# Optimization experiments

Measured on AMD Instinct MI355X. Metric: run time of the kernel, lower is better.

## Reference

```python
import jax, jax.numpy as jnp
import numpy as np

B, LQ, LD = 64, 20, 512
D, NB, WIN = 300, 11, 5
EQ, ED, DESC, KC = 5, 10, 20, 10
VW, VE, VC = 50000, 10000, 5000

# KNRM kernel centers / widths (requires_grad=False buffers in the original)
MU = jnp.array([1.0, 0.9, 0.7, 0.5, 0.3, 0.1, -0.1, -0.3, -0.5, -0.7, -0.9], jnp.float32)
SIGMA = jnp.array([1e-3] + [0.1] * 10, jnp.float32)


def setup_inputs() -> dict:
    key = jax.random.key(0)
    ks = jax.random.split(key, 20)
    f = lambda k, s, sc: jax.random.normal(k, s, jnp.float32) * sc
    return {
        "inputs_qwt": jax.random.randint(ks[0], (B, LQ), 0, VW),
        "inputs_qwm": jnp.ones((B, LQ), jnp.float32),
        "inputs_qei": jax.random.randint(ks[1], (B, EQ), 0, VE),
        "inputs_qet": jax.random.randint(ks[2], (B, EQ * DESC), 0, VW),
        "inputs_qew": jax.random.randint(ks[3], (B, EQ * KC), 0, VC),
        "inputs_qem": jnp.ones((B, EQ), jnp.float32),
        "inputs_dwt": jax.random.randint(ks[4], (B, LD), 0, VW),
        "inputs_dwm": jnp.ones((B, LD), jnp.float32),
        "inputs_dei": jax.random.randint(ks[5], (B, ED), 0, VE),
        "inputs_det": jax.random.randint(ks[6], (B, ED * DESC), 0, VW),
        "inputs_dew": jax.random.randint(ks[7], (B, ED * KC), 0, VC),
        "inputs_dem": jnp.ones((B, ED), jnp.float32),
        "wrd_emb": f(ks[8], (VW, D), 0.1),
        "ent_emb": f(ks[9], (VE, 128), 0.1),
        "car_emb": f(ks[10], (VC, 128), 0.1),
        "bow_W": f(ks[11], (128, D), 0.05), "bow_b": jnp.zeros((128,), jnp.float32),
        "conv_uni_W": f(ks[12], (128, 1, D), 0.05), "conv_uni_b": jnp.zeros((128,), jnp.float32),
        "conv_bi_W": f(ks[13], (128, 2, D), 0.04), "conv_bi_b": jnp.zeros((128,), jnp.float32),
        "conv_tri_W": f(ks[14], (128, 3, D), 0.03), "conv_tri_b": jnp.zeros((128,), jnp.float32),
        "conv_des_W": f(ks[15], (128, WIN, D), 0.02), "conv_des_b": jnp.zeros((128,), jnp.float32),
        "dense_f_W": f(ks[16], (1, 16 * NB), 0.1), "dense_f_b": jnp.zeros((1,), jnp.float32),
    }


def _conv_words(x, w, b):
    # x: [N, L, D]; w: [O, k, D] -> relu conv over the word axis, valid padding -> [N, L-k+1, O]
    k, L = w.shape[1], x.shape[1]
    segs = jnp.stack([x[:, i:L - k + 1 + i] for i in range(k)], axis=2)  # [N, L-k+1, k, D]
    return jax.nn.relu(jnp.einsum('nlkd,okd->nlo', segs, w) + b)


def _l2(x):
    return x / jnp.maximum(jnp.linalg.norm(x, axis=-1, keepdims=True), 1e-10)


def _kernel_pool(q, d, mq, md):
    # q:[B,Lq,128] d:[B,Ld,128] mq:[B,Lq] md:[B,Ld] -> [B, NB]
    sim = jnp.einsum('bqe,bde->bqd', q, d)
    pv = jnp.exp(-0.5 * (sim[..., None] - MU) ** 2 / (SIGMA ** 2)) * md[:, None, :, None]
    lps = jnp.log(jnp.maximum(pv.sum(2), 1e-10)) * 0.01 * mq[:, :, None]
    return lps.sum(1)


def _forward(inputs_qwt, inputs_qwm, inputs_qei, inputs_qet, inputs_qew, inputs_qem,
             inputs_dwt, inputs_dwm, inputs_dei, inputs_det, inputs_dew, inputs_dem,
             wrd_emb, ent_emb, car_emb, bow_W, bow_b,
             conv_uni_W, conv_uni_b, conv_bi_W, conv_bi_b, conv_tri_W, conv_tri_b,
             conv_des_W, conv_des_b, dense_f_W, dense_f_b):
    b = inputs_qwt.shape[0]
    qw = wrd_emb[inputs_qwt]  # [B, LQ, D]
    dw = wrd_emb[inputs_dwt]  # [B, LD, D]

    def ent_branch(ids_e, ids_desc, ids_car, n_ent, w_bow):
        desc = wrd_emb[ids_desc].reshape(b * n_ent, DESC, D)
        e_conv = _conv_words(desc, conv_des_W, conv_des_b).max(1).reshape(b, n_ent, 128)
        t = car_emb[ids_car].reshape(b, n_ent * KC, 128)
        att = jax.nn.softmax((w_bow * t).sum(2).reshape(b, n_ent, KC, 1), axis=2)
        ew = (att * t.reshape(b, n_ent, KC, 128)).sum(2)
        return ent_emb[ids_e] + e_conv + ew

    qw_bow = (jnp.einsum('bld,od->blo', qw, bow_W) + bow_b).sum(1, keepdims=True)  # [B,1,128]
    dw_bow = (jnp.einsum('bld,od->blo', dw, bow_W) + bow_b).sum(1, keepdims=True)
    qs = _l2(ent_branch(inputs_qei, inputs_qet, inputs_qew, EQ, qw_bow))  # [B,5,128]
    ds = _l2(ent_branch(inputs_dei, inputs_det, inputs_dew, ED, dw_bow))  # [B,10,128]

    qu = _l2(_conv_words(qw, conv_uni_W, conv_uni_b))
    qb = _l2(_conv_words(qw, conv_bi_W, conv_bi_b))
    qt = _l2(_conv_words(qw, conv_tri_W, conv_tri_b))
    du = _l2(_conv_words(dw, conv_uni_W, conv_uni_b))
    db = _l2(_conv_words(dw, conv_bi_W, conv_bi_b))
    dt = _l2(_conv_words(dw, conv_tri_W, conv_tri_b))

    mqu, mqb, mqt = inputs_qwm, inputs_qwm[:, :-1], inputs_qwm[:, :-2]
    mdu, mdb, mdt = inputs_dwm, inputs_dwm[:, :-1], inputs_dwm[:, :-2]

    kp = _kernel_pool
    pools = [kp(qu, du, mqu, mdu), kp(qu, dt, mqu, mdt), kp(qu, db, mqu, mdb),
             kp(qb, du, mqb, mdu), kp(qt, du, mqt, mdu), kp(qb, db, mqb, mdb),
             kp(qb, dt, mqb, mdt), kp(qt, db, mqt, mdb), kp(qt, dt, mqt, mdt),
             kp(qs, du, inputs_qem, mdu), kp(qs, db, inputs_qem, mdb), kp(qs, dt, inputs_qem, mdt),
             kp(qu, ds, mqu, inputs_dem), kp(qb, ds, mqb, inputs_dem), kp(qt, ds, mqt, inputs_dem),
             kp(qs, ds, inputs_qem, inputs_dem)]
    feats = jnp.concatenate(pools, axis=1)  # [B, 16*NB]
    return jnp.tanh(feats @ dense_f_W.T + dense_f_b)[:, 0]


def reference(inputs_qwt, inputs_qwm, inputs_qei, inputs_qet, inputs_qew, inputs_qem,
              inputs_dwt, inputs_dwm, inputs_dei, inputs_det, inputs_dew, inputs_dem,
              wrd_emb, ent_emb, car_emb, bow_W, bow_b,
              conv_uni_W, conv_uni_b, conv_bi_W, conv_bi_b, conv_tri_W, conv_tri_b,
              conv_des_W, conv_des_b, dense_f_W, dense_f_b):
    return _forward(inputs_qwt, inputs_qwm, inputs_qei, inputs_qet, inputs_qew, inputs_qem,
                    inputs_dwt, inputs_dwm, inputs_dei, inputs_det, inputs_dew, inputs_dem,
                    wrd_emb, ent_emb, car_emb, bow_W, bow_b,
                    conv_uni_W, conv_uni_b, conv_bi_W, conv_bi_b, conv_tri_W, conv_tri_b,
                    conv_des_W, conv_des_b, dense_f_W, dense_f_b)
```

## Files before the change

kernel.cpp:

```cpp
#include <hip/hip_runtime.h>

typedef unsigned short u16;
typedef unsigned int u32;
typedef __attribute__((ext_vector_type(8))) short bf16x8;
typedef __attribute__((ext_vector_type(4))) float f32x4;

#define DEVI __device__ __forceinline__

namespace {
constexpr int LQ_ = 20, LD_ = 512, D_ = 300;
constexpr int EQ_ = 5, ED_ = 10, KC_ = 10;
constexpr int QROWS = 62, DROWS = 1543;
constexpr int QSTR = 64, DSTR = 1600;
constexpr int XDOC0 = 0;
constexpr int XQ0   = 32768;
constexpr int XQD0  = 34048;
constexpr int XDD0  = 40448;
constexpr int XNR   = 53248;
constexpr float MU_H[11] = {1.0f,0.9f,0.7f,0.5f,0.3f,0.1f,-0.1f,-0.3f,-0.5f,-0.7f,-0.9f};
}

__constant__ int P2QT_C[16] = {0,0,0,1,2,1,1,2,2,3,3,3,0,1,2,3};
__constant__ int P2DT_C[16] = {0,2,1,0,0,1,2,1,2,0,1,2,3,3,3,3};
__constant__ int NP_C[4]   = {2,2,4,4};
__constant__ int PPL_C[16] = {0,1,0,0, 2,3,0,0, 2,3,4,5, 4,5,6,7};
__constant__ int SETL_C[16]= {0,0,0,0, 0,0,0,0, 1,1,0,0, 1,1,0,0};

DEVI u16 f2bf(float f){ union{float f;u32 u;} v; v.f=f; u32 r=(v.u+0x7fffu+((v.u>>16)&1u))>>16; return (u16)r; }
DEVI float bf2f(u16 h){ union{u32 u;float f;} v; v.u=((u32)h)<<16; return v.f; }

__global__ __launch_bounds__(256) void k_prep(const int* __restrict__ dwt, const int* __restrict__ qwt,
                                              const int* __restrict__ qet, const int* __restrict__ det,
                                              const float* __restrict__ emb, u16* __restrict__ xall,
                                              const float* __restrict__ Wu, const float* __restrict__ Wb,
                                              const float* __restrict__ Wt, const float* __restrict__ Wd,
                                              u16* __restrict__ Wp){
  const int bx = blockIdx.x;
  if(bx < 16640){
    long idx = (long)bx*256 + threadIdx.x;
    int row = (int)(idx/80), q = (int)(idx - (long)row*80);
    int tid;
    if(row < XQ0) tid = dwt[row];
    else if(row < XQD0) tid = qwt[row-XQ0];
    else if(row < XDD0) tid = qet[row-XQD0];
    else tid = det[row-XDD0];
    ushort4 o4;
    if(q < 75){
      float4 v = ((const float4*)(emb + (long)tid*D_))[q];
      o4.x=f2bf(v.x); o4.y=f2bf(v.y); o4.z=f2bf(v.z); o4.w=f2bf(v.w);
    } else { o4.x=0;o4.y=0;o4.z=0;o4.w=0; }
    *(ushort4*)(xall + (long)row*320 + q*4) = o4;
  } else {
    const int b2 = bx - 16640;
    const int ts = b2/10, ks = b2 - ts*10;
    const float* W; int kk, tap;
    if(ts==0){W=Wu;kk=1;tap=0;}
    else if(ts<3){W=Wb;kk=2;tap=ts-1;}
    else if(ts<6){W=Wt;kk=3;tap=ts-3;}
    else {W=Wd;kk=5;tap=ts-6;}
    for(int idx=threadIdx.x; idx<4096; idx+=256){
      int n0=idx>>9, lane=(idx>>3)&63, j=idx&7;
      int col=lane&15, kg=lane>>4;
      int d=ks*32+kg*8+j, o=n0*16+col;
      float v = (d<300)? W[((long)o*kk + tap)*300 + d] : 0.f;
      Wp[(((long)(ts*8+n0)*10+ks)*64 + lane)*8 + j] = f2bf(v);
    }
  }
}

__global__ __launch_bounds__(512) void k_main(const u16* __restrict__ xall, const u16* __restrict__ Wp,
    const float* __restrict__ bu, const float* __restrict__ bb, const float* __restrict__ bt,
    u16* __restrict__ dcat, u16* __restrict__ qcat, float* __restrict__ parts)
{
  __shared__ __align__(16) char smem[76576];
  const int bx = blockIdx.x, t = threadIdx.x;
  if(bx < 576){
    const bool isdoc = bx < 512;
    const int seq   = isdoc? (bx>>3) : (bx-512);
    const int l0    = isdoc? (bx&7)*64 : 0;
    const int Ltok  = isdoc? LD_ : LQ_;
    const int rowbase = isdoc? XDOC0 : XQ0;
    u16* outp = isdoc? dcat : qcat;
    const long seqstride = isdoc? (long)DSTR*128 : (long)QSTR*128;
    u16* xs = (u16*)smem;
    float* ot = (float*)(smem + 43296);
    const int nrows = min(66, Ltok - l0);
    const u16* src = xall + ((long)(rowbase + seq*Ltok + l0))*320;
    {
      const bf16x8 z = {0,0,0,0,0,0,0,0};
      for(int idx=t; idx<66*40; idx+=512){
        int r=idx/40, cc=idx-r*40;
        bf16x8 v = *(const bf16x8*)&src[(long)r*320 + cc*8];
        *(bf16x8*)&xs[r*328 + cc*8] = (r<nrows)? v : z;
      }
    }
    __syncthreads();
    const int lane=t&63, wave=t>>6;
    const int col16=lane&15, kg=lane>>4;
    #pragma unroll
    for(int c=0;c<3;c++){
      const int tb = (c==0)?0:((c==1)?1:3);
      const int base = (c==0)?0:((c==1)?Ltok:2*Ltok-1);
      const float* bias = (c==0)?bu:((c==1)?bb:bt);
      f32x4 acc4[4];
      #pragma unroll
      for(int mt=0;mt<4;mt++) acc4[mt]=(f32x4){0.f,0.f,0.f,0.f};
      #pragma unroll
      for(int h=0;h<2;h++){
        bf16x8 wf[15];
        #pragma unroll
        for(int i=0;i<=c;i++)
          #pragma unroll
          for(int k5=0;k5<5;k5++)
            wf[i*5+k5] = *(const bf16x8*)(Wp + (((long)((tb+i)*8 + wave)*10) + h*5 + k5)*512 + lane*8);
        #pragma unroll
        for(int mt=0;mt<4;mt++){
          #pragma unroll
          for(int i=0;i<=c;i++){
            const u16* xrow = &xs[(mt*16 + col16 + i)*328 + h*160];
            #pragma unroll
            for(int k5=0;k5<5;k5++){
              bf16x8 a = *(const bf16x8*)(xrow + k5*32 + kg*8);
              acc4[mt]=__builtin_amdgcn_mfma_f32_16x16x32_bf16(a,wf[i*5+k5],acc4[mt],0,0,0);
            }
          }
        }
      }
      const float bv = bias[wave*16+col16];
      #pragma unroll
      for(int mt=0;mt<4;mt++)
        #pragma unroll
        for(int reg=0;reg<4;reg++)
          ot[(mt*16+kg*4+reg)*130 + wave*16+col16] = fmaxf(acc4[mt][reg]+bv, 0.f);
      __syncthreads();
      {
        const int p = t>>3, j = t&7;
        const int nv = min(64, (Ltok - c) - l0);
        float ss=0.f;
        if(p<nv){
          #pragma unroll
          for(int k=0;k<16;k++){ float v = ot[p*130 + j + 8*k]; ss += v*v; }
        }
        ss += __shfl_xor(ss,1); ss += __shfl_xor(ss,2); ss += __shfl_xor(ss,4);
        if(p<nv){
          float inv = 1.0f/fmaxf(sqrtf(ss),1e-10f);
          u16* ob = outp + (long)seq*seqstride + ((long)(base + l0 + p))*128 + j*16;
          #pragma unroll
          for(int hh=0;hh<2;hh++){
            bf16x8 o8;
            #pragma unroll
            for(int e=0;e<8;e++) o8[e] = (short)f2bf(ot[p*130 + j*16 + hh*8 + e]*inv);
            *(bf16x8*)(ob + hh*8) = o8;
          }
        }
      }
      __syncthreads();
    }
  } else {
    const int idx = bx - 576;
    const int side = idx>>6, b = idx&63;
    const int q = t%80, g = t/80;
    if(g<6){
      float a0=0.f,a1=0.f,a2=0.f,a3=0.f;
      const int L = side? LD_ : LQ_;
      const long base = side? ((long)b*LD_)*320 : ((long)(XQ0 + b*LQ_))*320;
      for(int r=g; r<L; r+=6){
        ushort4 v = *(const ushort4*)(xall + base + (long)r*320 + q*4);
        a0+=bf2f(v.x); a1+=bf2f(v.y); a2+=bf2f(v.z); a3+=bf2f(v.w);
      }
      if(q<76){
        float4 o4={a0,a1,a2,a3};
        *(float4*)(parts + (((long)side*64 + b)*8 + g)*304 + q*4) = o4;
      }
    }
  }
}

__global__ __launch_bounds__(512) void k_desc(const u16* __restrict__ xall,
    const u16* __restrict__ Wp, const float* __restrict__ bd,
    float* __restrict__ qdm, float* __restrict__ ddm)
{
  const int t=threadIdx.x, lane=t&63, wave=t>>6;
  const int col16=lane&15, kg=lane>>4;
  const bool isq = blockIdx.x < 80;
  const int s0 = (isq? blockIdx.x : blockIdx.x-80)*4;
  const int rowbase = isq? XQD0 : XDD0;
  float* dm = isq? qdm : ddm;
  __shared__ u16 xs4[4*20*328];
  {
    for(int idx=t; idx<4*20*40; idx+=512){
      int s=idx/800, rem=idx-s*800, r=rem/40, cc=rem-r*40;
      *(bf16x8*)&xs4[(s*20+r)*328 + cc*8] =
        *(const bf16x8*)&xall[((long)(rowbase + (s0+s)*20 + r))*320 + cc*8];
    }
  }
  __syncthreads();
  f32x4 acc4[4];
  #pragma unroll
  for(int s=0;s<4;s++) acc4[s]=(f32x4){0.f,0.f,0.f,0.f};
  #pragma unroll
  for(int h=0;h<2;h++){
    bf16x8 wf[25];
    #pragma unroll
    for(int tap=0;tap<5;tap++)
      #pragma unroll
      for(int k5=0;k5<5;k5++)
        wf[tap*5+k5] = *(const bf16x8*)(Wp + (((long)((6+tap)*8 + wave)*10) + h*5 + k5)*512 + lane*8);
    #pragma unroll
    for(int s=0;s<4;s++){
      #pragma unroll
      for(int tap=0;tap<5;tap++){
        const u16* xrow = &xs4[(s*20 + col16 + tap)*328 + h*160];
        #pragma unroll
        for(int k5=0;k5<5;k5++){
          bf16x8 a = *(const bf16x8*)(xrow + k5*32 + kg*8);
          acc4[s]=__builtin_amdgcn_mfma_f32_16x16x32_bf16(a,wf[tap*5+k5],acc4[s],0,0,0);
        }
      }
    }
  }
  const float bv = bd[wave*16+col16];
  #pragma unroll
  for(int s=0;s<4;s++){
    float m=-1e30f;
    #pragma unroll
    for(int reg=0;reg<4;reg++) m=fmaxf(m, acc4[s][reg]+bv);
    m=fmaxf(m,__shfl_xor(m,16));
    m=fmaxf(m,__shfl_xor(m,32));
    m=fmaxf(m,0.f);
    if(kg==0) dm[(long)(s0+s)*128 + wave*16+col16]=m;
  }
}

__global__ __launch_bounds__(256) void k_entpost(
    const int* __restrict__ qei, const int* __restrict__ qew,
    const int* __restrict__ dei, const int* __restrict__ dew,
    const float* __restrict__ qdm, const float* __restrict__ ddm,
    const float* __restrict__ parts, const float* __restrict__ bowW, const float* __restrict__ bowb,
    const float* __restrict__ ent, const float* __restrict__ car,
    u16* __restrict__ qcat, u16* __restrict__ dcat)
{
  const int e15 = blockIdx.x, b = blockIdx.y, t = threadIdx.x;
  const bool isq = (e15 < EQ_);
  const int e = isq? e15 : e15-EQ_;
  const float* dmx = isq? (qdm + (long)(b*EQ_+e)*128) : (ddm + (long)(b*ED_+e)*128);
  const int eid = isq? qei[b*EQ_+e] : dei[b*ED_+e];
  const int* carids = isq? (qew + b*EQ_*KC_ + e*KC_) : (dew + b*ED_*KC_ + e*KC_);
  u16* orow = isq? (qcat + ((long)b*QSTR + 57 + e)*128) : (dcat + ((long)b*DSTR + 1533 + e)*128);

  __shared__ float carS[KC_*128];
  __shared__ float sv[304];
  __shared__ float bwS[128];
  __shared__ float sc[KC_], att[KC_];
  __shared__ float red[4];
  const float* p = parts + (((long)(isq?0:1)*64 + b)*8)*304;
  for(int d=t; d<304; d+=256){
    float s=0.f;
    #pragma unroll
    for(int g=0;g<6;g++) s += p[g*304+d];
    sv[d]=s;
  }
  for(int idx=t; idx<KC_*128; idx+=256){
    int j = idx>>7, c = idx&127;
    carS[j*128+c] = car[(long)carids[j]*128 + c];
  }
  __syncthreads();
  {
    const int ch = t>>1, h = t&1;
    float acc=0.f;
    const float* w = bowW + (long)ch*300 + h*150;
    const float* x = sv + h*150;
    for(int d=0; d<150; d++) acc += x[d]*w[d];
    acc += __shfl_xor(acc,1);
    if(h==0) bwS[ch] = acc + (isq? (float)LQ_ : (float)LD_)*bowb[ch];
  }
  __syncthreads();
  {
    const int j = t>>4, l16 = t&15;
    if(j < KC_){
      float s=0.f;
      for(int c=l16;c<128;c+=16) s += bwS[c]*carS[j*128+c];
      s += __shfl_xor(s,1); s += __shfl_xor(s,2); s += __shfl_xor(s,4); s += __shfl_xor(s,8);
      if(l16==0) sc[j]=s;
    }
  }
  __syncthreads();
  if(t==0){
    float m=-1e30f;
    for(int x=0;x<KC_;x++) m = fmaxf(m, sc[x]);
    float ssum=0.f;
    for(int x=0;x<KC_;x++){ float e2=__expf(sc[x]-m); att[x]=e2; ssum+=e2; }
    float rs = 1.0f/ssum;
    for(int x=0;x<KC_;x++) att[x]*=rs;
  }
  __syncthreads();
  float val=0.f;
  if(t<128){
    float ew=0.f;
    for(int x=0;x<KC_;x++) ew += att[x]*carS[x*128+t];
    val = ent[(long)eid*128+t] + dmx[t] + ew;
  }
  float ss = val*val;
  ss += __shfl_xor(ss,1); ss += __shfl_xor(ss,2); ss += __shfl_xor(ss,4);
  ss += __shfl_xor(ss,8); ss += __shfl_xor(ss,16); ss += __shfl_xor(ss,32);
  if((t&63)==0) red[t>>6]=ss;
  __syncthreads();
  if(t<128){
    float nv = 1.0f/fmaxf(sqrtf(red[0]+red[1]),1e-10f);
    orow[t] = f2bf(val*nv);
  }
}

__global__ __launch_bounds__(512) void k_simgauss(const u16* __restrict__ qcat, const u16* __restrict__ dcat,
                                                  const float* __restrict__ dwm, const float* __restrict__ dem,
                                                  float* __restrict__ Spart){
  const int b=blockIdx.x, piece=blockIdx.y;
  const int t=threadIdx.x, lane=t&63, wave=t>>6;
  const int qtile=wave>>1, dpar=wave&1;
  const int col16=lane&15, kg=lane>>4;
  constexpr int NT[4]={8,8,8,1};
  constexpr int TBASE[4]={0,8,16,24};
  constexpr int PEND[4]={512,1023,1533,1543};
  bf16x8 afr[4];
  #pragma unroll
  for(int ks=0;ks<4;ks++)
    afr[ks] = *(const bf16x8*)&qcat[((long)b*QSTR + qtile*16+col16)*128 + ks*32 + kg*8];
  float aP[4][11], aS[4][11];
  #pragma unroll
  for(int r=0;r<4;r++)
    #pragma unroll
    for(int m=0;m<11;m++){ aP[r][m]=0.f; aS[r][m]=0.f; }
  const int t0 = dpar*4;
  const int t1 = (NT[piece] < t0+4)? NT[piece] : t0+4;
  for(int tt=t0; tt<t1; tt++){
    const int tb = TBASE[piece]+tt;
    f32x4 acc[4];
    #pragma unroll
    for(int n0=0;n0<4;n0++) acc[n0]=(f32x4){0.f,0.f,0.f,0.f};
    #pragma unroll
    for(int ks=0;ks<4;ks++){
      #pragma unroll
      for(int n0=0;n0<4;n0++){
        bf16x8 bfr = *(const bf16x8*)&dcat[((long)b*DSTR + tb*64 + n0*16+col16)*128 + ks*32 + kg*8];
        acc[n0]=__builtin_amdgcn_mfma_f32_16x16x32_bf16(afr[ks],bfr,acc[n0],0,0,0);
      }
    }
    #pragma unroll
    for(int n0=0;n0<4;n0++){
      const int col = tb*64 + n0*16 + col16;
      float md;
      if(col<512) md = dwm[b*LD_+col];
      else if(col<1023) md = dwm[b*LD_+col-512];
      else if(col<1533) md = dwm[b*LD_+col-1023];
      else if(col<1543) md = dem[b*ED_+(col-1533)];
      else md = 0.f;
      const bool pr = col < PEND[piece];
      const float mdP = pr? md : 0.f;
      const float mdS = pr? 0.f : md;
      #pragma unroll
      for(int reg=0;reg<4;reg++){
        const float svv = acc[n0][reg];
        {
          float d1 = svv-1.0f;
          float e = __expf(-500000.0f*d1*d1);
          aP[reg][0] += mdP*e; aS[reg][0] += mdS*e;
        }
        #pragma unroll
        for(int m=1;m<11;m++){
          float dm = svv-MU_H[m];
          float e = __expf(-50.0f*dm*dm);
          aP[reg][m] += mdP*e; aS[reg][m] += mdS*e;
        }
      }
    }
  }
  #pragma unroll
  for(int reg=0;reg<4;reg++)
    #pragma unroll
    for(int m=0;m<11;m++){
      float vP=aP[reg][m];
      vP+=__shfl_xor(vP,1); vP+=__shfl_xor(vP,2); vP+=__shfl_xor(vP,4); vP+=__shfl_xor(vP,8);
      aP[reg][m]=vP;
      float vS=aS[reg][m];
      vS+=__shfl_xor(vS,1); vS+=__shfl_xor(vS,2); vS+=__shfl_xor(vS,4); vS+=__shfl_xor(vS,8);
      aS[reg][m]=vS;
    }
  if(col16==0){
    #pragma unroll
    for(int reg=0;reg<4;reg++){
      const int qr = qtile*16 + kg*4 + reg;
      float* o = Spart + (((long)b*64 + qr)*8 + piece*2+dpar)*22;
      #pragma unroll
      for(int m=0;m<11;m++){ o[m]=aP[reg][m]; o[11+m]=aS[reg][m]; }
    }
  }
}

__global__ __launch_bounds__(256) void k_feats(const float* __restrict__ Spart, const float* __restrict__ qwm,
                                               const float* __restrict__ qem, const float* __restrict__ dfW,
                                               const float* __restrict__ dfb, float* __restrict__ out){
  const int b = blockIdx.x, t = threadIdx.x;
  __shared__ float fsh[176];
  __shared__ float red[4];
  if(t<176){
    const int pool = t/11, m = t - pool*11;
    const int qt = P2QT_C[pool], dt = P2DT_C[pool];
    const int qlo = (qt==0)?0:((qt==1)?20:((qt==2)?39:57));
    const int qn  = (qt==0)?20:((qt==1)?19:((qt==2)?18:5));
    float f = 0.f;
    for(int r=0;r<qn;r++){
      const int qr = qlo + r;
      float mq = (qt<3)? qwm[b*LQ_+r] : qem[b*EQ_+r];
      const float* row = Spart + (((long)b*64 + qr)*8)*22 + m;
      float sv = 0.f;
      const int np = NP_C[dt];
      for(int k=0;k<np;k++){
        const int ii = dt*4+k;
        sv += row[PPL_C[ii]*22 + SETL_C[ii]*11];
      }
      f += logf(fmaxf(sv,1e-10f))*0.01f*mq;
    }
    fsh[t] = f;
  }
  __syncthreads();
  float v = (t<176)? fsh[t]*dfW[t] : 0.f;
  v += __shfl_xor(v,1); v += __shfl_xor(v,2); v += __shfl_xor(v,4);
  v += __shfl_xor(v,8); v += __shfl_xor(v,16); v += __shfl_xor(v,32);
  if((t&63)==0) red[t>>6]=v;
  __syncthreads();
  if(t==0) out[b] = tanhf(red[0]+red[1]+red[2]+red[3] + dfb[0]);
}

extern "C" void kernel_launch(void* const* d_in, const int* in_sizes, int n_in,
                              void* d_out, int out_size, void* d_ws, size_t ws_size,
                              hipStream_t stream)
{
  const int*   qwt=(const int*)d_in[0];
  const float* qwm=(const float*)d_in[1];
  const int*   qei=(const int*)d_in[2];
  const int*   qet=(const int*)d_in[3];
  const int*   qew=(const int*)d_in[4];
  const float* qem=(const float*)d_in[5];
  const int*   dwt=(const int*)d_in[6];
  const float* dwm=(const float*)d_in[7];
  const int*   dei=(const int*)d_in[8];
  const int*   det=(const int*)d_in[9];
  const int*   dew=(const int*)d_in[10];
  const float* dem=(const float*)d_in[11];
  const float* emb=(const float*)d_in[12];
  const float* ent=(const float*)d_in[13];
  const float* car=(const float*)d_in[14];
  const float* bowW=(const float*)d_in[15];
  const float* bowb=(const float*)d_in[16];
  const float* Wu=(const float*)d_in[17];
  const float* bu=(const float*)d_in[18];
  const float* Wb=(const float*)d_in[19];
  const float* bb=(const float*)d_in[20];
  const float* Wt=(const float*)d_in[21];
  const float* bt=(const float*)d_in[22];
  const float* Wd=(const float*)d_in[23];
  const float* bd=(const float*)d_in[24];
  const float* dfW=(const float*)d_in[25];
  const float* dfb=(const float*)d_in[26];
  float* out=(float*)d_out;

  char* ws=(char*)d_ws;
  size_t off=0;
  auto A=[&](size_t n){ size_t r=off; off=(off+n+255)&~(size_t)255; return r; };
  u16* Wp     = (u16*)(ws + A((size_t)11*8*10*64*8*2));
  u16* dcat   = (u16*)(ws + A((size_t)64*DSTR*128*2));
  u16* qcat   = (u16*)(ws + A((size_t)64*QSTR*128*2));
  float* qdm  = (float*)(ws + A((size_t)320*128*4));
  float* ddm  = (float*)(ws + A((size_t)640*128*4));
  float* parts= (float*)(ws + A((size_t)2*64*8*304*4));
  float* Spart= (float*)(ws + A((size_t)64*64*8*22*4));
  u16*   xall = (u16*)(ws + A((size_t)XNR*320*2));
  if(off > ws_size) return;

  k_prep<<<16750,256,0,stream>>>(dwt,qwt,qet,det,emb,xall,Wu,Wb,Wt,Wd,Wp);
  k_main<<<704,512,0,stream>>>(xall,Wp,bu,bb,bt,dcat,qcat,parts);
  k_desc<<<240,512,0,stream>>>(xall,Wp,bd,qdm,ddm);
  k_entpost<<<dim3(15,64),256,0,stream>>>(qei,qew,dei,dew,qdm,ddm,parts,bowW,bowb,ent,car,qcat,dcat);
  k_simgauss<<<dim3(64,4),512,0,stream>>>(qcat,dcat,dwm,dem,Spart);
  k_feats<<<64,256,0,stream>>>(Spart,qwm,qem,dfW,dfb,out);
}
```

Baseline: 176.4 us.

## Fuse embedding gather into conv kernels and merge similarity with feature pooling

Removes the separate bf16 embedding staging buffer: the conv, description-conv and bag-of-words blocks now gather and convert embedding rows directly from the fp32 table into shared memory, and k_desc is folded into k_main as extra blocks. The similarity/gaussian kernel and the feature kernel are merged, with per-batch partials kept in shared memory instead of a global buffer. This cuts kernel launches and global round trips. In exchange the similarity stage runs on 64 blocks instead of 256, which lowers parallelism, and the gathers now read fp32 rows with less coalescing. The ot row stride also changes from 130 to 132.

New measurement: 245.0 us. 1.39x slower.

```diff
diff --git a/kernel.cpp b/kernel.cpp
--- a/kernel.cpp
+++ b/kernel.cpp
@@ -12,11 +12,6 @@
 constexpr int EQ_ = 5, ED_ = 10, KC_ = 10;
 constexpr int QROWS = 62, DROWS = 1543;
 constexpr int QSTR = 64, DSTR = 1600;
-constexpr int XDOC0 = 0;
-constexpr int XQ0   = 32768;
-constexpr int XQD0  = 34048;
-constexpr int XDD0  = 40448;
-constexpr int XNR   = 53248;
 constexpr float MU_H[11] = {1.0f,0.9f,0.7f,0.5f,0.3f,0.1f,-0.1f,-0.3f,-0.5f,-0.7f,-0.9f};
 }
 
@@ -29,74 +24,59 @@
 DEVI u16 f2bf(float f){ union{float f;u32 u;} v; v.f=f; u32 r=(v.u+0x7fffu+((v.u>>16)&1u))>>16; return (u16)r; }
 DEVI float bf2f(u16 h){ union{u32 u;float f;} v; v.u=((u32)h)<<16; return v.f; }
 
-__global__ __launch_bounds__(256) void k_prep(const int* __restrict__ dwt, const int* __restrict__ qwt,
-                                              const int* __restrict__ qet, const int* __restrict__ det,
-                                              const float* __restrict__ emb, u16* __restrict__ xall,
-                                              const float* __restrict__ Wu, const float* __restrict__ Wb,
-                                              const float* __restrict__ Wt, const float* __restrict__ Wd,
-                                              u16* __restrict__ Wp){
-  const int bx = blockIdx.x;
-  if(bx < 16640){
-    long idx = (long)bx*256 + threadIdx.x;
-    int row = (int)(idx/80), q = (int)(idx - (long)row*80);
-    int tid;
-    if(row < XQ0) tid = dwt[row];
-    else if(row < XQD0) tid = qwt[row-XQ0];
-    else if(row < XDD0) tid = qet[row-XQD0];
-    else tid = det[row-XDD0];
-    ushort4 o4;
-    if(q < 75){
-      float4 v = ((const float4*)(emb + (long)tid*D_))[q];
-      o4.x=f2bf(v.x); o4.y=f2bf(v.y); o4.z=f2bf(v.z); o4.w=f2bf(v.w);
-    } else { o4.x=0;o4.y=0;o4.z=0;o4.w=0; }
-    *(ushort4*)(xall + (long)row*320 + q*4) = o4;
-  } else {
-    const int b2 = bx - 16640;
-    const int ts = b2/10, ks = b2 - ts*10;
-    const float* W; int kk, tap;
-    if(ts==0){W=Wu;kk=1;tap=0;}
-    else if(ts<3){W=Wb;kk=2;tap=ts-1;}
-    else if(ts<6){W=Wt;kk=3;tap=ts-3;}
-    else {W=Wd;kk=5;tap=ts-6;}
-    for(int idx=threadIdx.x; idx<4096; idx+=256){
-      int n0=idx>>9, lane=(idx>>3)&63, j=idx&7;
-      int col=lane&15, kg=lane>>4;
-      int d=ks*32+kg*8+j, o=n0*16+col;
-      float v = (d<300)? W[((long)o*kk + tap)*300 + d] : 0.f;
-      Wp[(((long)(ts*8+n0)*10+ks)*64 + lane)*8 + j] = f2bf(v);
-    }
-  }
-}
-
-__global__ __launch_bounds__(512) void k_main(const u16* __restrict__ xall, const u16* __restrict__ Wp,
+__global__ __launch_bounds__(256) void k_wpack(const float* __restrict__ Wu, const float* __restrict__ Wb,
+                                               const float* __restrict__ Wt, const float* __restrict__ Wd,
+                                               u16* __restrict__ Wp){
+  const int ts = blockIdx.x/10, ks = blockIdx.x%10;
+  const float* W; int kk, tap;
+  if(ts==0){W=Wu;kk=1;tap=0;}
+  else if(ts<3){W=Wb;kk=2;tap=ts-1;}
+  else if(ts<6){W=Wt;kk=3;tap=ts-3;}
+  else {W=Wd;kk=5;tap=ts-6;}
+  for(int idx=threadIdx.x; idx<4096; idx+=256){
+    int n0=idx>>9, lane=(idx>>3)&63, j=idx&7;
+    int col=lane&15, kg=lane>>4;
+    int d=ks*32+kg*8+j, o=n0*16+col;
+    float v = (d<300)? W[((long)o*kk + tap)*300 + d] : 0.f;
+    Wp[(((long)(ts*8+n0)*10+ks)*64 + lane)*8 + j] = f2bf(v);
+  }
+}
+
+__global__ __launch_bounds__(512) void k_main(
+    const int* __restrict__ dwt, const int* __restrict__ qwt,
+    const int* __restrict__ qet, const int* __restrict__ det,
+    const float* __restrict__ emb, const u16* __restrict__ Wp,
     const float* __restrict__ bu, const float* __restrict__ bb, const float* __restrict__ bt,
-    u16* __restrict__ dcat, u16* __restrict__ qcat, float* __restrict__ parts)
+    const float* __restrict__ bd,
+    u16* __restrict__ dcat, u16* __restrict__ qcat,
+    float* __restrict__ qdm, float* __restrict__ ddm, float* __restrict__ parts)
 {
-  __shared__ __align__(16) char smem[76576];
+  __shared__ __align__(16) char smem[77088];
+  __shared__ int tokid[80];
   const int bx = blockIdx.x, t = threadIdx.x;
+  const int lane=t&63, wave=t>>6, col16=lane&15, kg=lane>>4;
   if(bx < 576){
     const bool isdoc = bx < 512;
     const int seq   = isdoc? (bx>>3) : (bx-512);
     const int l0    = isdoc? (bx&7)*64 : 0;
     const int Ltok  = isdoc? LD_ : LQ_;
-    const int rowbase = isdoc? XDOC0 : XQ0;
     u16* outp = isdoc? dcat : qcat;
     const long seqstride = isdoc? (long)DSTR*128 : (long)QSTR*128;
     u16* xs = (u16*)smem;
     float* ot = (float*)(smem + 43296);
     const int nrows = min(66, Ltok - l0);
-    const u16* src = xall + ((long)(rowbase + seq*Ltok + l0))*320;
-    {
-      const bf16x8 z = {0,0,0,0,0,0,0,0};
-      for(int idx=t; idx<66*40; idx+=512){
-        int r=idx/40, cc=idx-r*40;
-        bf16x8 v = *(const bf16x8*)&src[(long)r*320 + cc*8];
-        *(bf16x8*)&xs[r*328 + cc*8] = (r<nrows)? v : z;
-      }
-    }
+    if(t<66) tokid[t] = (t<nrows)? (isdoc? dwt[seq*LD_+l0+t] : qwt[seq*LQ_+t]) : 0;
     __syncthreads();
-    const int lane=t&63, wave=t>>6;
-    const int col16=lane&15, kg=lane>>4;
+    for(int idx=t; idx<66*80; idx+=512){
+      int r=idx/80, q=idx-r*80;
+      ushort4 o4;
+      if(q<75 && r<nrows){
+        float4 v = ((const float4*)(emb + (long)tokid[r]*D_))[q];
+        o4.x=f2bf(v.x); o4.y=f2bf(v.y); o4.z=f2bf(v.z); o4.w=f2bf(v.w);
+      } else { o4.x=0;o4.y=0;o4.z=0;o4.w=0; }
+      *(ushort4*)&xs[r*328 + q*4] = o4;
+    }
+    __syncthreads();
     #pragma unroll
     for(int c=0;c<3;c++){
       const int tb = (c==0)?0:((c==1)?1:3);
@@ -117,10 +97,10 @@
         for(int mt=0;mt<4;mt++){
           #pragma unroll
           for(int i=0;i<=c;i++){
-            const u16* xrow = &xs[(mt*16 + col16 + i)*328 + h*160];
+            const u16* xrow = &xs[(mt*16 + col16 + i)*328 + h*160 + kg*8];
             #pragma unroll
             for(int k5=0;k5<5;k5++){
-              bf16x8 a = *(const bf16x8*)(xrow + k5*32 + kg*8);
+              bf16x8 a = *(const bf16x8*)(xrow + k5*32);
               acc4[mt]=__builtin_amdgcn_mfma_f32_16x16x32_bf16(a,wf[i*5+k5],acc4[mt],0,0,0);
             }
           }
@@ -131,7 +111,7 @@
       for(int mt=0;mt<4;mt++)
         #pragma unroll
         for(int reg=0;reg<4;reg++)
-          ot[(mt*16+kg*4+reg)*130 + wave*16+col16] = fmaxf(acc4[mt][reg]+bv, 0.f);
+          ot[(mt*16+kg*4+reg)*132 + wave*16+col16] = fmaxf(acc4[mt][reg]+bv, 0.f);
       __syncthreads();
       {
         const int p = t>>3, j = t&7;
@@ -139,7 +119,7 @@
         float ss=0.f;
         if(p<nv){
           #pragma unroll
-          for(int k=0;k<16;k++){ float v = ot[p*130 + j + 8*k]; ss += v*v; }
+          for(int k=0;k<16;k++){ float v = ot[p*132 + j + 8*k]; ss += v*v; }
         }
         ss += __shfl_xor(ss,1); ss += __shfl_xor(ss,2); ss += __shfl_xor(ss,4);
         if(p<nv){
@@ -149,86 +129,86 @@
           for(int hh=0;hh<2;hh++){
             bf16x8 o8;
             #pragma unroll
-            for(int e=0;e<8;e++) o8[e] = (short)f2bf(ot[p*130 + j*16 + hh*8 + e]*inv);
+            for(int e=0;e<8;e++) o8[e] = (short)f2bf(ot[p*132 + j*16 + hh*8 + e]*inv);
             *(bf16x8*)(ob + hh*8) = o8;
           }
         }
       }
       __syncthreads();
     }
+  } else if(bx < 816){
+    const int d = bx - 576;
+    const bool isq = d < 80;
+    const int s0 = (isq? d : d-80)*4;
+    const int* dt_ = isq? qet : det;
+    float* dm = isq? qdm : ddm;
+    u16* xs4 = (u16*)smem;
+    if(t<80) tokid[t] = dt_[s0*20 + t];
+    __syncthreads();
+    for(int idx=t; idx<80*80; idx+=512){
+      int lr=idx/80, q=idx-lr*80;
+      ushort4 o4;
+      if(q<75){
+        float4 v = ((const float4*)(emb + (long)tokid[lr]*D_))[q];
+        o4.x=f2bf(v.x); o4.y=f2bf(v.y); o4.z=f2bf(v.z); o4.w=f2bf(v.w);
+      } else { o4.x=0;o4.y=0;o4.z=0;o4.w=0; }
+      *(ushort4*)&xs4[lr*328 + q*4] = o4;
+    }
+    __syncthreads();
+    f32x4 acc4[4];
+    #pragma unroll
+    for(int s=0;s<4;s++) acc4[s]=(f32x4){0.f,0.f,0.f,0.f};
+    #pragma unroll
+    for(int h=0;h<2;h++){
+      bf16x8 wf[25];
+      #pragma unroll
+      for(int tap=0;tap<5;tap++)
+        #pragma unroll
+        for(int k5=0;k5<5;k5++)
+          wf[tap*5+k5] = *(const bf16x8*)(Wp + (((long)((6+tap)*8 + wave)*10) + h*5 + k5)*512 + lane*8);
+      #pragma unroll
+      for(int s=0;s<4;s++){
+        #pragma unroll
+        for(int tap=0;tap<5;tap++){
+          const u16* xrow = &xs4[(s*20 + col16 + tap)*328 + h*160 + kg*8];
+          #pragma unroll
+          for(int k5=0;k5<5;k5++){
+            bf16x8 a = *(const bf16x8*)(xrow + k5*32);
+            acc4[s]=__builtin_amdgcn_mfma_f32_16x16x32_bf16(a,wf[tap*5+k5],acc4[s],0,0,0);
+          }
+        }
+      }
+    }
+    const float bv = bd[wave*16+col16];
+    #pragma unroll
+    for(int s=0;s<4;s++){
+      float m=-1e30f;
+      #pragma unroll
+      for(int reg=0;reg<4;reg++) m=fmaxf(m, acc4[s][reg]+bv);
+      m=fmaxf(m,__shfl_xor(m,16));
+      m=fmaxf(m,__shfl_xor(m,32));
+      m=fmaxf(m,0.f);
+      if(kg==0) dm[(long)(s0+s)*128 + wave*16+col16]=m;
+    }
   } else {
-    const int idx = bx - 576;
+    const int idx = bx - 816;
     const int side = idx>>6, b = idx&63;
     const int q = t%80, g = t/80;
     if(g<6){
       float a0=0.f,a1=0.f,a2=0.f,a3=0.f;
       const int L = side? LD_ : LQ_;
-      const long base = side? ((long)b*LD_)*320 : ((long)(XQ0 + b*LQ_))*320;
-      for(int r=g; r<L; r+=6){
-        ushort4 v = *(const ushort4*)(xall + base + (long)r*320 + q*4);
-        a0+=bf2f(v.x); a1+=bf2f(v.y); a2+=bf2f(v.z); a3+=bf2f(v.w);
+      if(q<75){
+        for(int r=g; r<L; r+=6){
+          const int tok = side? dwt[b*LD_+r] : qwt[b*LQ_+r];
+          float4 v = ((const float4*)(emb + (long)tok*D_))[q];
+          a0+=v.x; a1+=v.y; a2+=v.z; a3+=v.w;
+        }
       }
       if(q<76){
         float4 o4={a0,a1,a2,a3};
         *(float4*)(parts + (((long)side*64 + b)*8 + g)*304 + q*4) = o4;
       }
     }
-  }
-}
-
-__global__ __launch_bounds__(512) void k_desc(const u16* __restrict__ xall,
-    const u16* __restrict__ Wp, const float* __restrict__ bd,
-    float* __restrict__ qdm, float* __restrict__ ddm)
-{
-  const int t=threadIdx.x, lane=t&63, wave=t>>6;
-  const int col16=lane&15, kg=lane>>4;
-  const bool isq = blockIdx.x < 80;
-  const int s0 = (isq? blockIdx.x : blockIdx.x-80)*4;
-  const int rowbase = isq? XQD0 : XDD0;
-  float* dm = isq? qdm : ddm;
-  __shared__ u16 xs4[4*20*328];
-  {
-    for(int idx=t; idx<4*20*40; idx+=512){
-      int s=idx/800, rem=idx-s*800, r=rem/40, cc=rem-r*40;
-      *(bf16x8*)&xs4[(s*20+r)*328 + cc*8] =
-        *(const bf16x8*)&xall[((long)(rowbase + (s0+s)*20 + r))*320 + cc*8];
-    }
-  }
-  __syncthreads();
-  f32x4 acc4[4];
-  #pragma unroll
-  for(int s=0;s<4;s++) acc4[s]=(f32x4){0.f,0.f,0.f,0.f};
-  #pragma unroll
-  for(int h=0;h<2;h++){
-    bf16x8 wf[25];
-    #pragma unroll
-    for(int tap=0;tap<5;tap++)
-      #pragma unroll
-      for(int k5=0;k5<5;k5++)
-        wf[tap*5+k5] = *(const bf16x8*)(Wp + (((long)((6+tap)*8 + wave)*10) + h*5 + k5)*512 + lane*8);
-    #pragma unroll
-    for(int s=0;s<4;s++){
-      #pragma unroll
-      for(int tap=0;tap<5;tap++){
-        const u16* xrow = &xs4[(s*20 + col16 + tap)*328 + h*160];
-        #pragma unroll
-        for(int k5=0;k5<5;k5++){
-          bf16x8 a = *(const bf16x8*)(xrow + k5*32 + kg*8);
-          acc4[s]=__builtin_amdgcn_mfma_f32_16x16x32_bf16(a,wf[tap*5+k5],acc4[s],0,0,0);
-        }
-      }
-    }
-  }
-  const float bv = bd[wave*16+col16];
-  #pragma unroll
-  for(int s=0;s<4;s++){
-    float m=-1e30f;
-    #pragma unroll
-    for(int reg=0;reg<4;reg++) m=fmaxf(m, acc4[s][reg]+bv);
-    m=fmaxf(m,__shfl_xor(m,16));
-    m=fmaxf(m,__shfl_xor(m,32));
-    m=fmaxf(m,0.f);
-    if(kg==0) dm[(long)(s0+s)*128 + wave*16+col16]=m;
   }
 }
 
@@ -311,97 +291,97 @@
   }
 }
 
-__global__ __launch_bounds__(512) void k_simgauss(const u16* __restrict__ qcat, const u16* __restrict__ dcat,
+__global__ __launch_bounds__(512) void k_simfeats(const u16* __restrict__ qcat, const u16* __restrict__ dcat,
                                                   const float* __restrict__ dwm, const float* __restrict__ dem,
-                                                  float* __restrict__ Spart){
-  const int b=blockIdx.x, piece=blockIdx.y;
+                                                  const float* __restrict__ qwm, const float* __restrict__ qem,
+                                                  const float* __restrict__ dfW, const float* __restrict__ dfb,
+                                                  float* __restrict__ out){
+  const int b=blockIdx.x;
   const int t=threadIdx.x, lane=t&63, wave=t>>6;
-  const int qtile=wave>>1, dpar=wave&1;
+  const int piece=wave>>1, dpar=wave&1;
   const int col16=lane&15, kg=lane>>4;
   constexpr int NT[4]={8,8,8,1};
   constexpr int TBASE[4]={0,8,16,24};
   constexpr int PEND[4]={512,1023,1533,1543};
-  bf16x8 afr[4];
-  #pragma unroll
-  for(int ks=0;ks<4;ks++)
-    afr[ks] = *(const bf16x8*)&qcat[((long)b*QSTR + qtile*16+col16)*128 + ks*32 + kg*8];
-  float aP[4][11], aS[4][11];
-  #pragma unroll
-  for(int r=0;r<4;r++)
-    #pragma unroll
-    for(int m=0;m<11;m++){ aP[r][m]=0.f; aS[r][m]=0.f; }
+  __shared__ float Sl[64*8*22];
+  __shared__ float fsh[176];
+  __shared__ float red[4];
   const int t0 = dpar*4;
   const int t1 = (NT[piece] < t0+4)? NT[piece] : t0+4;
-  for(int tt=t0; tt<t1; tt++){
-    const int tb = TBASE[piece]+tt;
-    f32x4 acc[4];
-    #pragma unroll
-    for(int n0=0;n0<4;n0++) acc[n0]=(f32x4){0.f,0.f,0.f,0.f};
-    #pragma unroll
-    for(int ks=0;ks<4;ks++){
+  for(int qtile=0;qtile<4;qtile++){
+    bf16x8 afr[4];
+    #pragma unroll
+    for(int ks=0;ks<4;ks++)
+      afr[ks] = *(const bf16x8*)&qcat[((long)b*QSTR + qtile*16+col16)*128 + ks*32 + kg*8];
+    float aP[4][11], aS[4][11];
+    #pragma unroll
+    for(int r=0;r<4;r++)
+      #pragma unroll
+      for(int m=0;m<11;m++){ aP[r][m]=0.f; aS[r][m]=0.f; }
+    for(int tt=t0; tt<t1; tt++){
+      const int tb = TBASE[piece]+tt;
+      f32x4 acc[4];
+      #pragma unroll
+      for(int n0=0;n0<4;n0++) acc[n0]=(f32x4){0.f,0.f,0.f,0.f};
+      #pragma unroll
+      for(int ks=0;ks<4;ks++){
+        #pragma unroll
+        for(int n0=0;n0<4;n0++){
+          bf16x8 bfr = *(const bf16x8*)&dcat[((long)b*DSTR + tb*64 + n0*16+col16)*128 + ks*32 + kg*8];
+          acc[n0]=__builtin_amdgcn_mfma_f32_16x16x32_bf16(afr[ks],bfr,acc[n0],0,0,0);
+        }
+      }
       #pragma unroll
       for(int n0=0;n0<4;n0++){
-        bf16x8 bfr = *(const bf16x8*)&dcat[((long)b*DSTR + tb*64 + n0*16+col16)*128 + ks*32 + kg*8];
-        acc[n0]=__builtin_amdgcn_mfma_f32_16x16x32_bf16(afr[ks],bfr,acc[n0],0,0,0);
-      }
-    }
-    #pragma unroll
-    for(int n0=0;n0<4;n0++){
-      const int col = tb*64 + n0*16 + col16;
-      float md;
-      if(col<512) md = dwm[b*LD_+col];
-      else if(col<1023) md = dwm[b*LD_+col-512];
-      else if(col<1533) md = dwm[b*LD_+col-1023];
-      else if(col<1543) md = dem[b*ED_+(col-1533)];
-      else md = 0.f;
-      const bool pr = col < PEND[piece];
-      const float mdP = pr? md : 0.f;
-      const float mdS = pr? 0.f : md;
+        const int col = tb*64 + n0*16 + col16;
+        float md;
+        if(col<512) md = dwm[b*LD_+col];
+        else if(col<1023) md = dwm[b*LD_+col-512];
+        else if(col<1533) md = dwm[b*LD_+col-1023];
+        else if(col<1543) md = dem[b*ED_+(col-1533)];
+        else md = 0.f;
+        const bool pr = col < PEND[piece];
+        const float mdP = pr? md : 0.f;
+        const float mdS = pr? 0.f : md;
+        #pragma unroll
+        for(int reg=0;reg<4;reg++){
+          const float svv = acc[n0][reg];
+          {
+            float d1 = svv-1.0f;
+            float e = __expf(-500000.0f*d1*d1);
+            aP[reg][0] += mdP*e; aS[reg][0] += mdS*e;
+          }
+          #pragma unroll
+          for(int m=1;m<11;m++){
+            float dm = svv-MU_H[m];
+            float e = __expf(-50.0f*dm*dm);
+            aP[reg][m] += mdP*e; aS[reg][m] += mdS*e;
+          }
+        }
+      }
+    }
+    #pragma unroll
+    for(int reg=0;reg<4;reg++)
+      #pragma unroll
+      for(int m=0;m<11;m++){
+        float vP=aP[reg][m];
+        vP+=__shfl_xor(vP,1); vP+=__shfl_xor(vP,2); vP+=__shfl_xor(vP,4); vP+=__shfl_xor(vP,8);
+        aP[reg][m]=vP;
+        float vS=aS[reg][m];
+        vS+=__shfl_xor(vS,1); vS+=__shfl_xor(vS,2); vS+=__shfl_xor(vS,4); vS+=__shfl_xor(vS,8);
+        aS[reg][m]=vS;
+      }
+    if(col16==0){
       #pragma unroll
       for(int reg=0;reg<4;reg++){
-        const float svv = acc[n0][reg];
-        {
-          float d1 = svv-1.0f;
-          float e = __expf(-500000.0f*d1*d1);
-          aP[reg][0] += mdP*e; aS[reg][0] += mdS*e;
-        }
-        #pragma unroll
-        for(int m=1;m<11;m++){
-          float dm = svv-MU_H[m];
-          float e = __expf(-50.0f*dm*dm);
-          aP[reg][m] += mdP*e; aS[reg][m] += mdS*e;
-        }
-      }
-    }
-  }
-  #pragma unroll
-  for(int reg=0;reg<4;reg++)
-    #pragma unroll
-    for(int m=0;m<11;m++){
-      float vP=aP[reg][m];
-      vP+=__shfl_xor(vP,1); vP+=__shfl_xor(vP,2); vP+=__shfl_xor(vP,4); vP+=__shfl_xor(vP,8);
-      aP[reg][m]=vP;
-      float vS=aS[reg][m];
-      vS+=__shfl_xor(vS,1); vS+=__shfl_xor(vS,2); vS+=__shfl_xor(vS,4); vS+=__shfl_xor(vS,8);
-      aS[reg][m]=vS;
-    }
-  if(col16==0){
-    #pragma unroll
-    for(int reg=0;reg<4;reg++){
-      const int qr = qtile*16 + kg*4 + reg;
-      float* o = Spart + (((long)b*64 + qr)*8 + piece*2+dpar)*22;
-      #pragma unroll
-      for(int m=0;m<11;m++){ o[m]=aP[reg][m]; o[11+m]=aS[reg][m]; }
-    }
-  }
-}
-
-__global__ __launch_bounds__(256) void k_feats(const float* __restrict__ Spart, const float* __restrict__ qwm,
-                                               const float* __restrict__ qem, const float* __restrict__ dfW,
-                                               const float* __restrict__ dfb, float* __restrict__ out){
-  const int b = blockIdx.x, t = threadIdx.x;
-  __shared__ float fsh[176];
-  __shared__ float red[4];
+        const int qr = qtile*16 + kg*4 + reg;
+        float* o = Sl + ((long)qr*8 + piece*2+dpar)*22;
+        #pragma unroll
+        for(int m=0;m<11;m++){ o[m]=aP[reg][m]; o[11+m]=aS[reg][m]; }
+      }
+    }
+  }
+  __syncthreads();
   if(t<176){
     const int pool = t/11, m = t - pool*11;
     const int qt = P2QT_C[pool], dt = P2DT_C[pool];
@@ -411,7 +391,7 @@
     for(int r=0;r<qn;r++){
       const int qr = qlo + r;
       float mq = (qt<3)? qwm[b*LQ_+r] : qem[b*EQ_+r];
-      const float* row = Spart + (((long)b*64 + qr)*8)*22 + m;
+      const float* row = Sl + (long)qr*8*22 + m;
       float sv = 0.f;
       const int np = NP_C[dt];
       for(int k=0;k<np;k++){
@@ -473,14 +453,10 @@
   float* qdm  = (float*)(ws + A((size_t)320*128*4));
   float* ddm  = (float*)(ws + A((size_t)640*128*4));
   float* parts= (float*)(ws + A((size_t)2*64*8*304*4));
-  float* Spart= (float*)(ws + A((size_t)64*64*8*22*4));
-  u16*   xall = (u16*)(ws + A((size_t)XNR*320*2));
   if(off > ws_size) return;
 
-  k_prep<<<16750,256,0,stream>>>(dwt,qwt,qet,det,emb,xall,Wu,Wb,Wt,Wd,Wp);
-  k_main<<<704,512,0,stream>>>(xall,Wp,bu,bb,bt,dcat,qcat,parts);
-  k_desc<<<240,512,0,stream>>>(xall,Wp,bd,qdm,ddm);
+  k_wpack<<<110,256,0,stream>>>(Wu,Wb,Wt,Wd,Wp);
+  k_main<<<944,512,0,stream>>>(dwt,qwt,qet,det,emb,Wp,bu,bb,bt,bd,dcat,qcat,qdm,ddm,parts);
   k_entpost<<<dim3(15,64),256,0,stream>>>(qei,qew,dei,dew,qdm,ddm,parts,bowW,bowb,ent,car,qcat,dcat);
-  k_simgauss<<<dim3(64,4),512,0,stream>>>(qcat,dcat,dwm,dem,Spart);
-  k_feats<<<64,256,0,stream>>>(Spart,qwm,qem,dfW,dfb,out);
-}
+  k_simfeats<<<64,512,0,stream>>>(qcat,dcat,dwm,dem,qwm,qem,dfW,dfb,out);
+}
```
